# Kernel tuning notes

Measured on AMD Instinct MI355X. Metric: run time of the kernel, lower is better.

## Reference

```python
import jax, jax.numpy as jnp
import numpy as np

HEADS = 16
EMB_DIM = 1024
MODEL_DIM = 1024
HEAD_DIM = EMB_DIM // HEADS
N, SEQ = 4, 1024


def setup_inputs() -> dict:
    key = jax.random.key(0)
    ks = jax.random.split(key, 9)
    s = 1.0 / np.sqrt(EMB_DIM)
    return {
        "query_inputs": jax.random.normal(ks[0], (N, SEQ, EMB_DIM), jnp.float32),
        "key_inputs": jax.random.normal(ks[1], (N, SEQ, EMB_DIM), jnp.float32),
        "value_inputs": jax.random.normal(ks[2], (N, SEQ, EMB_DIM), jnp.float32),
        "Wq": jax.random.normal(ks[3], (MODEL_DIM, EMB_DIM), jnp.float32) * s,
        "bq": jax.random.normal(ks[4], (MODEL_DIM,), jnp.float32) * s,
        "Wk": jax.random.normal(ks[5], (MODEL_DIM, EMB_DIM), jnp.float32) * s,
        "bk": jax.random.normal(ks[6], (MODEL_DIM,), jnp.float32) * s,
        "Wv": jax.random.normal(ks[7], (MODEL_DIM, EMB_DIM), jnp.float32) * s,
        "bv": jax.random.normal(ks[8], (MODEL_DIM,), jnp.float32) * s,
    }


def reference(query_inputs, key_inputs, value_inputs, Wq, bq, Wk, bk, Wv, bv):
    n = query_inputs.shape[0]
    qi = query_inputs.reshape(n, -1, query_inputs.shape[-1])
    ki = key_inputs.reshape(n, -1, key_inputs.shape[-1])
    vi = value_inputs.reshape(n, -1, value_inputs.shape[-1])
    q = qi @ Wq.T + bq  # (n, L, model_dim)
    k = ki @ Wk.T + bk
    v = vi @ Wv.T + bv
    L = q.shape[1]
    # Faithful to original (q/v swapped role): 'values'<-q, 'queries'<-v
    values = q.reshape(n, L, HEADS, HEAD_DIM)
    keys = k.reshape(n, L, HEADS, HEAD_DIM)
    queries = v.reshape(n, L, HEADS, HEAD_DIM)
    energy = jnp.einsum('nqhd,nkhd->nhqk', queries, keys)
    attention = jax.nn.softmax(energy / jnp.sqrt(jnp.float32(EMB_DIM)), axis=3)
    out = jnp.einsum('nhql,nlhd->nqhd', attention, values).reshape(n, L, HEADS * HEAD_DIM)
    return out
```

## Files before the change

### kernel.cpp

```cpp
#include <hip/hip_runtime.h>


typedef unsigned short u16;
typedef __attribute__((ext_vector_type(8))) short bf16x8;
typedef __attribute__((ext_vector_type(4))) float f32x4;

#define S_LEN 1024
#define EMB 1024
#define HEADS 16
#define HD 64

__device__ __forceinline__ u16 f2bf(float f) {
    unsigned int u = __float_as_uint(f);
    u = (u + 0x7fffu + ((u >> 16) & 1u)) >> 16;
    return (u16)u;
}

__global__ __launch_bounds__(256) void qkv_gemm(
    const float* __restrict__ Xq, const float* __restrict__ Xk, const float* __restrict__ Xv,
    const float* __restrict__ Wq, const float* __restrict__ Wk, const float* __restrict__ Wv,
    const float* __restrict__ Bq, const float* __restrict__ Bk, const float* __restrict__ Bv,
    u16* __restrict__ vt, u16* __restrict__ katt, u16* __restrict__ qatt)
{
    const int proj = blockIdx.z;
    const float* X = (proj == 0) ? Xq : (proj == 1) ? Xk : Xv;
    const float* W = (proj == 0) ? Wq : (proj == 1) ? Wk : Wv;
    const float* Bp = (proj == 0) ? Bq : (proj == 1) ? Bk : Bv;

    const int gm0 = blockIdx.x * 128;
    const int gn0 = blockIdx.y * 128;
    const int tid  = threadIdx.x;
    const int lane = tid & 63;
    const int wave = tid >> 6;
    const int wm = wave >> 1, wn = wave & 1;
    const int l15 = lane & 15, l4 = lane >> 4;

    __shared__ u16 As[128 * 40];
    __shared__ u16 Bs[128 * 40];

    f32x4 acc[4][4];
    #pragma unroll
    for (int i = 0; i < 4; ++i)
        #pragma unroll
        for (int j = 0; j < 4; ++j) {
            f32x4 z = {0.f, 0.f, 0.f, 0.f};
            acc[i][j] = z;
        }

    const int srow = tid >> 3;
    const int skc  = (tid & 7) * 4;

    for (int kt = 0; kt < 32; ++kt) {
        const int k0 = kt * 32;
        #pragma unroll
        for (int p = 0; p < 4; ++p) {
            const int row = p * 32 + srow;
            float4 a = *reinterpret_cast<const float4*>(&X[(size_t)(gm0 + row) * EMB + k0 + skc]);
            float4 b = *reinterpret_cast<const float4*>(&W[(size_t)(gn0 + row) * EMB + k0 + skc]);
            ushort4 ua; ua.x = f2bf(a.x); ua.y = f2bf(a.y); ua.z = f2bf(a.z); ua.w = f2bf(a.w);
            ushort4 ub; ub.x = f2bf(b.x); ub.y = f2bf(b.y); ub.z = f2bf(b.z); ub.w = f2bf(b.w);
            *reinterpret_cast<ushort4*>(&As[row * 40 + skc]) = ua;
            *reinterpret_cast<ushort4*>(&Bs[row * 40 + skc]) = ub;
        }
        __syncthreads();

        bf16x8 af[4], bfr[4];
        #pragma unroll
        for (int m = 0; m < 4; ++m)
            af[m] = *reinterpret_cast<const bf16x8*>(&As[(wm * 64 + m * 16 + l15) * 40 + l4 * 8]);
        #pragma unroll
        for (int n = 0; n < 4; ++n)
            bfr[n] = *reinterpret_cast<const bf16x8*>(&Bs[(wn * 64 + n * 16 + l15) * 40 + l4 * 8]);

        #pragma unroll
        for (int m = 0; m < 4; ++m)
            #pragma unroll
            for (int n = 0; n < 4; ++n)
                acc[m][n] = __builtin_amdgcn_mfma_f32_16x16x32_bf16(af[m], bfr[n], acc[m][n], 0, 0, 0);
        __syncthreads();
    }

    #pragma unroll
    for (int n = 0; n < 4; ++n) {
        const int col = gn0 + wn * 64 + n * 16 + l15;
        const float bias = Bp[col];
        const int h = col >> 6, d = col & 63;
        #pragma unroll
        for (int m = 0; m < 4; ++m) {
            #pragma unroll
            for (int r = 0; r < 4; ++r) {
                const int rowg = gm0 + wm * 64 + m * 16 + l4 * 4 + r;
                const int nb = rowg >> 10, s = rowg & 1023;
                const u16 val = f2bf(acc[m][n][r] + bias);
                const int nh = nb * HEADS + h;
                if (proj == 0)       vt  [((size_t)nh * HD + d) * S_LEN + s] = val;
                else if (proj == 1)  katt[((size_t)nh * S_LEN + s) * HD + d] = val;
                else                 qatt[((size_t)nh * S_LEN + s) * HD + d] = val;
            }
        }
    }
}

__global__ __launch_bounds__(256) void attn_kernel(
    const u16* __restrict__ qatt, const u16* __restrict__ katt,
    const u16* __restrict__ vt, float* __restrict__ out)
{
    const int qb = blockIdx.x;
    const int nh = blockIdx.y;
    const int tid  = threadIdx.x;
    const int lane = tid & 63;
    const int wave = tid >> 6;
    const int l15 = lane & 15, l4 = lane >> 4;
    const int q0 = qb * 64;
    const int waveQ = wave * 16;

    __shared__ u16 Ks[64 * 64];
    __shared__ u16 Vs[64 * 64];
    __shared__ u16 Ps[4 * 16 * 72];

    const size_t qbase = (size_t)nh * S_LEN * HD + (size_t)(q0 + waveQ + l15) * HD;
    const bf16x8 qf0 = *reinterpret_cast<const bf16x8*>(&qatt[qbase + l4 * 8]);
    const bf16x8 qf1 = *reinterpret_cast<const bf16x8*>(&qatt[qbase + 32 + l4 * 8]);

    f32x4 accO[4];
    #pragma unroll
    for (int i = 0; i < 4; ++i) { f32x4 z = {0.f,0.f,0.f,0.f}; accO[i] = z; }
    float m_run[4] = {-1e30f, -1e30f, -1e30f, -1e30f};
    float l_run[4] = {0.f, 0.f, 0.f, 0.f};
    const float scale = 0.03125f;

    char* KsB = reinterpret_cast<char*>(Ks);
    char* VsB = reinterpret_cast<char*>(Vs);

    for (int kt = 0; kt < 16; ++kt) {
        const size_t kbase = (size_t)nh * S_LEN * HD + (size_t)kt * 64 * HD;
        const size_t vbase = (size_t)nh * HD * S_LEN + (size_t)kt * 64;
        #pragma unroll
        for (int p = 0; p < 2; ++p) {
            const int cl  = tid + p * 256;
            const int row = cl >> 3, cc = cl & 7;
            const int dst = row * 128 + ((cc ^ (row & 7)) << 4);
            uint4 kv = *reinterpret_cast<const uint4*>(&katt[kbase + (size_t)cl * 8]);
            *reinterpret_cast<uint4*>(KsB + dst) = kv;
            uint4 vv = *reinterpret_cast<const uint4*>(&vt[vbase + (size_t)row * S_LEN + cc * 8]);
            *reinterpret_cast<uint4*>(VsB + dst) = vv;
        }
        __syncthreads();

        float pvals[4][4];
        #pragma unroll
        for (int kb = 0; kb < 4; ++kb) {
            const int krow = kb * 16 + l15;
            const int sw = krow & 7;
            bf16x8 kf0 = *reinterpret_cast<const bf16x8*>(KsB + krow * 128 + ((l4 ^ sw) << 4));
            bf16x8 kf1 = *reinterpret_cast<const bf16x8*>(KsB + krow * 128 + (((l4 + 4) ^ sw) << 4));
            f32x4 sacc = {0.f, 0.f, 0.f, 0.f};
            sacc = __builtin_amdgcn_mfma_f32_16x16x32_bf16(qf0, kf0, sacc, 0, 0, 0);
            sacc = __builtin_amdgcn_mfma_f32_16x16x32_bf16(qf1, kf1, sacc, 0, 0, 0);
            #pragma unroll
            for (int r = 0; r < 4; ++r) pvals[kb][r] = sacc[r] * scale;
        }

        float alpha[4];
        #pragma unroll
        for (int r = 0; r < 4; ++r) {
            float tmax = fmaxf(fmaxf(pvals[0][r], pvals[1][r]), fmaxf(pvals[2][r], pvals[3][r]));
            #pragma unroll
            for (int msk = 1; msk < 16; msk <<= 1) tmax = fmaxf(tmax, __shfl_xor(tmax, msk));
            const float mnew = fmaxf(m_run[r], tmax);
            alpha[r] = __expf(m_run[r] - mnew);
            float psum = 0.f;
            #pragma unroll
            for (int kb = 0; kb < 4; ++kb) {
                const float pv = __expf(pvals[kb][r] - mnew);
                pvals[kb][r] = pv;
                psum += pv;
            }
            #pragma unroll
            for (int msk = 1; msk < 16; msk <<= 1) psum += __shfl_xor(psum, msk);
            l_run[r] = l_run[r] * alpha[r] + psum;
            m_run[r] = mnew;
        }
        #pragma unroll
        for (int db = 0; db < 4; ++db) {
            f32x4 t = accO[db];
            t[0] *= alpha[0]; t[1] *= alpha[1]; t[2] *= alpha[2]; t[3] *= alpha[3];
            accO[db] = t;
        }

        u16* pw = &Ps[wave * 16 * 72];
        #pragma unroll
        for (int r = 0; r < 4; ++r) {
            const int prow = l4 * 4 + r;
            #pragma unroll
            for (int kb = 0; kb < 4; ++kb)
                pw[prow * 72 + kb * 16 + l15] = f2bf(pvals[kb][r]);
        }
        asm volatile("s_waitcnt lgkmcnt(0)" ::: "memory");
        __builtin_amdgcn_sched_barrier(0);

        const u16* pr = &Ps[wave * 16 * 72 + l15 * 72];
        const bf16x8 pf0 = *reinterpret_cast<const bf16x8*>(&pr[l4 * 8]);
        const bf16x8 pf1 = *reinterpret_cast<const bf16x8*>(&pr[32 + l4 * 8]);

        #pragma unroll
        for (int db = 0; db < 4; ++db) {
            const int vrow = db * 16 + l15;
            const int sw = vrow & 7;
            bf16x8 vf0 = *reinterpret_cast<const bf16x8*>(VsB + vrow * 128 + ((l4 ^ sw) << 4));
            bf16x8 vf1 = *reinterpret_cast<const bf16x8*>(VsB + vrow * 128 + (((l4 + 4) ^ sw) << 4));
            accO[db] = __builtin_amdgcn_mfma_f32_16x16x32_bf16(pf0, vf0, accO[db], 0, 0, 0);
            accO[db] = __builtin_amdgcn_mfma_f32_16x16x32_bf16(pf1, vf1, accO[db], 0, 0, 0);
        }
        __syncthreads();
    }

    const int n = nh >> 4, h = nh & 15;
    #pragma unroll
    for (int db = 0; db < 4; ++db) {
        const int d = h * 64 + db * 16 + l15;
        #pragma unroll
        for (int r = 0; r < 4; ++r) {
            const int s = q0 + waveQ + l4 * 4 + r;
            out[(size_t)n * S_LEN * EMB + (size_t)s * EMB + d] = accO[db][r] / l_run[r];
        }
    }
}

extern "C" void kernel_launch(void* const* d_in, const int* in_sizes, int n_in,
                              void* d_out, int out_size, void* d_ws, size_t ws_size,
                              hipStream_t stream)
{
    const float* Xq = (const float*)d_in[0];
    const float* Xk = (const float*)d_in[1];
    const float* Xv = (const float*)d_in[2];
    const float* Wq = (const float*)d_in[3];
    const float* bq = (const float*)d_in[4];
    const float* Wk = (const float*)d_in[5];
    const float* bk = (const float*)d_in[6];
    const float* Wv = (const float*)d_in[7];
    const float* bv = (const float*)d_in[8];
    float* out = (float*)d_out;

    u16* vt   = (u16*)d_ws;
    u16* katt = vt   + (size_t)4 * 1024 * 1024;
    u16* qatt = katt + (size_t)4 * 1024 * 1024;

    qkv_gemm<<<dim3(32, 8, 3), 256, 0, stream>>>(Xq, Xk, Xv, Wq, Wk, Wv, bq, bk, bv,
                                                 vt, katt, qatt);
    attn_kernel<<<dim3(16, 64), 256, 0, stream>>>(qatt, katt, vt, out);
}
```

Measured before the change: 223.2 us.

## Pre-convert QKV inputs and weights to bf16, load GEMM tiles via global_load_lds

Adds a grid-stride kernel that converts the three activation tensors and three weight matrices to bf16 in workspace. A new QKV GEMM consumes these bf16 copies and loads tiles straight into LDS with global_load_lds, which removes the per-tile fp32 loads and per-element rounding from the GEMM inner loop. The trade-off is an extra full pass over the fp32 inputs, more workspace, and unpadded LDS tiles that may cause bank conflicts. The old fp32 GEMM remains as a fallback when the workspace is too small.

```diff
diff --git a/kernel.cpp b/kernel.cpp
--- a/kernel.cpp
+++ b/kernel.cpp
@@ -16,15 +16,40 @@
     return (u16)u;
 }
 
-__global__ __launch_bounds__(256) void qkv_gemm(
-    const float* __restrict__ Xq, const float* __restrict__ Xk, const float* __restrict__ Xv,
-    const float* __restrict__ Wq, const float* __restrict__ Wk, const float* __restrict__ Wv,
+typedef const __attribute__((address_space(1))) unsigned glob_u32;
+typedef __attribute__((address_space(3))) unsigned lds_u32;
+__device__ __forceinline__ void gld16(const u16* g, u16* l) {
+    __builtin_amdgcn_global_load_lds((glob_u32*)g, (lds_u32*)l, 16, 0, 0);
+}
+
+struct CvtArgs {
+    const float* src[6];
+    u16* dst[6];
+};
+
+__global__ __launch_bounds__(256) void cvt_f32_bf16(CvtArgs a)
+{
+    const long total = (3L << 20) + (3L << 18);
+    for (long i = (long)blockIdx.x * 256 + threadIdx.x; i < total;
+         i += (long)gridDim.x * 256) {
+        int arr, off;
+        if (i < (3L << 20)) { arr = (int)(i >> 20); off = (int)(i & ((1 << 20) - 1)); }
+        else { long j = i - (3L << 20); arr = 3 + (int)(j >> 18); off = (int)(j & ((1 << 18) - 1)); }
+        float4 v = reinterpret_cast<const float4*>(a.src[arr])[off];
+        ushort4 o; o.x = f2bf(v.x); o.y = f2bf(v.y); o.z = f2bf(v.z); o.w = f2bf(v.w);
+        reinterpret_cast<ushort4*>(a.dst[arr])[off] = o;
+    }
+}
+
+__global__ __launch_bounds__(256) void qkv_gemm_bf16(
+    const u16* __restrict__ Xq, const u16* __restrict__ Xk, const u16* __restrict__ Xv,
+    const u16* __restrict__ Wq, const u16* __restrict__ Wk, const u16* __restrict__ Wv,
     const float* __restrict__ Bq, const float* __restrict__ Bk, const float* __restrict__ Bv,
     u16* __restrict__ vt, u16* __restrict__ katt, u16* __restrict__ qatt)
 {
     const int proj = blockIdx.z;
-    const float* X = (proj == 0) ? Xq : (proj == 1) ? Xk : Xv;
-    const float* W = (proj == 0) ? Wq : (proj == 1) ? Wk : Wv;
+    const u16* X  = (proj == 0) ? Xq : (proj == 1) ? Xk : Xv;
+    const u16* W  = (proj == 0) ? Wq : (proj == 1) ? Wk : Wv;
     const float* Bp = (proj == 0) ? Bq : (proj == 1) ? Bk : Bv;
 
     const int gm0 = blockIdx.x * 128;
@@ -35,6 +60,90 @@
     const int wm = wave >> 1, wn = wave & 1;
     const int l15 = lane & 15, l4 = lane >> 4;
 
+    __shared__ u16 As[128 * 32];
+    __shared__ u16 Bs[128 * 32];
+
+    f32x4 acc[4][4];
+    #pragma unroll
+    for (int i = 0; i < 4; ++i)
+        #pragma unroll
+        for (int j = 0; j < 4; ++j) { f32x4 z = {0.f,0.f,0.f,0.f}; acc[i][j] = z; }
+
+    const int r0 = tid >> 2,        cc0 = tid & 3;
+    const int r1 = (tid + 256) >> 2, cc1 = (tid + 256) & 3;
+    const u16* gA0 = X + (size_t)(gm0 + r0) * EMB + cc0 * 8;
+    const u16* gA1 = X + (size_t)(gm0 + r1) * EMB + cc1 * 8;
+    const u16* gB0 = W + (size_t)(gn0 + r0) * EMB + cc0 * 8;
+    const u16* gB1 = W + (size_t)(gn0 + r1) * EMB + cc1 * 8;
+    u16* lA0 = As + wave * 512;
+    u16* lA1 = As + 2048 + wave * 512;
+    u16* lB0 = Bs + wave * 512;
+    u16* lB1 = Bs + 2048 + wave * 512;
+
+    for (int kt = 0; kt < 32; ++kt) {
+        const int k0 = kt * 32;
+        gld16(gA0 + k0, lA0);
+        gld16(gA1 + k0, lA1);
+        gld16(gB0 + k0, lB0);
+        gld16(gB1 + k0, lB1);
+        __syncthreads();
+
+        bf16x8 af[4], bfr[4];
+        #pragma unroll
+        for (int m = 0; m < 4; ++m)
+            af[m] = *reinterpret_cast<const bf16x8*>(&As[(wm * 64 + m * 16 + l15) * 32 + l4 * 8]);
+        #pragma unroll
+        for (int n = 0; n < 4; ++n)
+            bfr[n] = *reinterpret_cast<const bf16x8*>(&Bs[(wn * 64 + n * 16 + l15) * 32 + l4 * 8]);
+
+        #pragma unroll
+        for (int m = 0; m < 4; ++m)
+            #pragma unroll
+            for (int n = 0; n < 4; ++n)
+                acc[m][n] = __builtin_amdgcn_mfma_f32_16x16x32_bf16(af[m], bfr[n], acc[m][n], 0, 0, 0);
+        __syncthreads();
+    }
+
+    #pragma unroll
+    for (int n = 0; n < 4; ++n) {
+        const int col = gn0 + wn * 64 + n * 16 + l15;
+        const float bias = Bp[col];
+        const int h = col >> 6, d = col & 63;
+        #pragma unroll
+        for (int m = 0; m < 4; ++m) {
+            #pragma unroll
+            for (int r = 0; r < 4; ++r) {
+                const int rowg = gm0 + wm * 64 + m * 16 + l4 * 4 + r;
+                const int nb = rowg >> 10, s = rowg & 1023;
+                const u16 val = f2bf(acc[m][n][r] + bias);
+                const int nh = nb * HEADS + h;
+                if (proj == 0)       vt  [((size_t)nh * HD + d) * S_LEN + s] = val;
+                else if (proj == 1)  katt[((size_t)nh * S_LEN + s) * HD + d] = val;
+                else                 qatt[((size_t)nh * S_LEN + s) * HD + d] = val;
+            }
+        }
+    }
+}
+
+__global__ __launch_bounds__(256) void qkv_gemm_f32(
+    const float* __restrict__ Xq, const float* __restrict__ Xk, const float* __restrict__ Xv,
+    const float* __restrict__ Wq, const float* __restrict__ Wk, const float* __restrict__ Wv,
+    const float* __restrict__ Bq, const float* __restrict__ Bk, const float* __restrict__ Bv,
+    u16* __restrict__ vt, u16* __restrict__ katt, u16* __restrict__ qatt)
+{
+    const int proj = blockIdx.z;
+    const float* X = (proj == 0) ? Xq : (proj == 1) ? Xk : Xv;
+    const float* W = (proj == 0) ? Wq : (proj == 1) ? Wk : Wv;
+    const float* Bp = (proj == 0) ? Bq : (proj == 1) ? Bk : Bv;
+
+    const int gm0 = blockIdx.x * 128;
+    const int gn0 = blockIdx.y * 128;
+    const int tid  = threadIdx.x;
+    const int lane = tid & 63;
+    const int wave = tid >> 6;
+    const int wm = wave >> 1, wn = wave & 1;
+    const int l15 = lane & 15, l4 = lane >> 4;
+
     __shared__ u16 As[128 * 40];
     __shared__ u16 Bs[128 * 40];
 
@@ -42,10 +151,7 @@
     #pragma unroll
     for (int i = 0; i < 4; ++i)
         #pragma unroll
-        for (int j = 0; j < 4; ++j) {
-            f32x4 z = {0.f, 0.f, 0.f, 0.f};
-            acc[i][j] = z;
-        }
+        for (int j = 0; j < 4; ++j) { f32x4 z = {0.f,0.f,0.f,0.f}; acc[i][j] = z; }
 
     const int srow = tid >> 3;
     const int skc  = (tid & 7) * 4;
@@ -242,11 +348,36 @@
     const float* bv = (const float*)d_in[8];
     float* out = (float*)d_out;
 
+    const size_t M4 = (size_t)4 * 1024 * 1024;
+    const size_t M1 = (size_t)1024 * 1024;
+
     u16* vt   = (u16*)d_ws;
-    u16* katt = vt   + (size_t)4 * 1024 * 1024;
-    u16* qatt = katt + (size_t)4 * 1024 * 1024;
-
-    qkv_gemm<<<dim3(32, 8, 3), 256, 0, stream>>>(Xq, Xk, Xv, Wq, Wk, Wv, bq, bk, bv,
-                                                 vt, katt, qatt);
+    u16* katt = vt + M4;
+    u16* qatt = katt + M4;
+
+    const size_t need = (3 * M4 + 3 * M4 + 3 * M1) * sizeof(u16);
+
+    if (ws_size >= need) {
+        u16* Xqb = qatt + M4;
+        u16* Xkb = Xqb + M4;
+        u16* Xvb = Xkb + M4;
+        u16* Wqb = Xvb + M4;
+        u16* Wkb = Wqb + M1;
+        u16* Wvb = Wkb + M1;
+
+        CvtArgs ca;
+        ca.src[0] = Xq; ca.src[1] = Xk; ca.src[2] = Xv;
+        ca.src[3] = Wq; ca.src[4] = Wk; ca.src[5] = Wv;
+        ca.dst[0] = Xqb; ca.dst[1] = Xkb; ca.dst[2] = Xvb;
+        ca.dst[3] = Wqb; ca.dst[4] = Wkb; ca.dst[5] = Wvb;
+        cvt_f32_bf16<<<2048, 256, 0, stream>>>(ca);
+
+        qkv_gemm_bf16<<<dim3(32, 8, 3), 256, 0, stream>>>(
+            Xqb, Xkb, Xvb, Wqb, Wkb, Wvb, bq, bk, bv, vt, katt, qatt);
+    } else {
+        qkv_gemm_f32<<<dim3(32, 8, 3), 256, 0, stream>>>(
+            Xq, Xk, Xv, Wq, Wk, Wv, bq, bk, bv, vt, katt, qatt);
+    }
+
     attn_kernel<<<dim3(16, 64), 256, 0, stream>>>(qatt, katt, vt, out);
 }
```

New measurement: 210.8 us. -5.6%, faster.
